# Performance work log

Measured on AMD Instinct MI355X. Metric: run time of the kernel, lower is better.

The kernel has to match this reference:

```python
import jax, jax.numpy as jnp
import numpy as np

V, E, H, K, B, T = 50000, 256, 512, 12, 32, 256
START, STOP = 10, 11
NEG = -10000.0
Hd = H // 2


def _lstm(x, h0, c0, Wih, Whh, bih, bhh):
    # x: [T, B, D] -> hidden states [T, B, Hd]; PyTorch gate order i,f,g,o
    def step(carry, xt):
        h, c = carry
        g = xt @ Wih.T + bih + h @ Whh.T + bhh
        i, f, gg, o = jnp.split(g, 4, axis=-1)
        c = jax.nn.sigmoid(f) * c + jax.nn.sigmoid(i) * jnp.tanh(gg)
        h = jax.nn.sigmoid(o) * jnp.tanh(c)
        return (h, c), h
    _, hs = jax.lax.scan(step, (h0, c0), x)
    return hs


def setup_inputs() -> dict:
    key = jax.random.key(0)
    ks = jax.random.split(key, 12)
    inp = {}
    inp["sentence"] = jax.random.randint(ks[0], (B, T), 0, V, dtype=jnp.int32)
    lens = jax.random.randint(ks[1], (B,), 1, T + 1, dtype=jnp.int32)
    inp["seq_lens"] = jnp.sort(lens)[::-1]  # pack_padded requires descending
    emb = jax.random.normal(ks[2], (V, E)) * 0.05
    inp["emb"] = emb.at[0].set(0.0)  # padding_idx=0
    def lw(k):
        a, b, c, d = jax.random.split(k, 4)
        return (jax.random.normal(a, (4 * Hd, E)) * 0.05,
                jax.random.normal(b, (4 * Hd, Hd)) * 0.05,
                jax.random.normal(c, (4 * Hd,)) * 0.05,
                jax.random.normal(d, (4 * Hd,)) * 0.05)
    inp["Wih_f"], inp["Whh_f"], inp["bih_f"], inp["bhh_f"] = lw(ks[3])
    inp["Wih_b"], inp["Whh_b"], inp["bih_b"], inp["bhh_b"] = lw(ks[4])
    inp["h0"] = jax.random.normal(ks[5], (2, B, Hd))  # init_hidden uses randn
    inp["c0"] = jax.random.normal(ks[6], (2, B, Hd))
    inp["W_out"] = jax.random.normal(ks[7], (K, H)) * 0.05
    inp["b_out"] = jax.random.normal(ks[8], (K,)) * 0.05
    trans = jax.random.normal(ks[9], (K, K))
    inp["transitions"] = trans.at[START, :].set(NEG).at[:, STOP].set(NEG)
    return inp


def _features(sentence, seq_lens, emb, Wih_f, Whh_f, bih_f, bhh_f,
              Wih_b, Whh_b, bih_b, bhh_b, h0, c0, W_out, b_out):
    x = emb[sentence]                       # [B,T,E]
    t_idx = jnp.arange(T)
    # forward direction
    hf = _lstm(x.transpose(1, 0, 2), h0[0], c0[0], Wih_f, Whh_f, bih_f, bhh_f)
    hf = hf.transpose(1, 0, 2)              # [B,T,Hd]
    # backward direction: reverse each sequence within its length (packed semantics)
    rev_idx = jnp.where(t_idx[None, :] < seq_lens[:, None],
                        seq_lens[:, None] - 1 - t_idx[None, :], t_idx[None, :])  # [B,T]
    x_rev = jnp.take_along_axis(x, rev_idx[:, :, None], axis=1)
    hb_rev = _lstm(x_rev.transpose(1, 0, 2), h0[1], c0[1], Wih_b, Whh_b, bih_b, bhh_b)
    hb = jnp.take_along_axis(hb_rev.transpose(1, 0, 2), rev_idx[:, :, None], axis=1)
    hcat = jnp.concatenate([hf, hb], axis=-1)  # [B,T,H]
    return hcat @ W_out.T + b_out              # [B,T,K]


def _viterbi(feats, seq_lens, transitions):
    t_idx = jnp.arange(T)
    mask = t_idx[None, :] < seq_lens[:, None]           # [B,T]
    init = jnp.full((B, K), NEG).at[:, START].set(0.0)  # forward_var

    def vstep(fv, inputs):
        feat_t, m_t = inputs                            # [B,K], [B]
        scores = fv[:, None, :] + transitions[None, :, :]   # [B, next, prev]
        bp = jnp.argmax(scores, axis=-1)                # [B,K]
        best = jnp.max(scores, axis=-1) + feat_t
        return jnp.where(m_t[:, None], best, fv), bp

    fv, bps = jax.lax.scan(vstep, init, (feats.transpose(1, 0, 2), mask.T))
    terminal = fv + transitions[STOP][None, :]          # [B,K]
    best_last = jnp.argmax(terminal, axis=-1)           # [B]
    path_scores = jnp.take_along_axis(terminal, best_last[:, None], axis=1)[:, 0]

    def btstep(tag, inputs):
        bp_t, m_t = inputs
        pred_t = jnp.where(m_t, tag, -1)
        prev = jnp.take_along_axis(bp_t, tag[:, None], axis=1)[:, 0]
        return jnp.where(m_t, prev, tag), pred_t

    _, preds_rev = jax.lax.scan(btstep, best_last, (bps[::-1], mask.T[::-1]))
    preds = preds_rev[::-1].transpose(1, 0)             # [B,T], -1 past seq_len
    return path_scores, preds


def reference(sentence, seq_lens, emb, Wih_f, Whh_f, bih_f, bhh_f,
              Wih_b, Whh_b, bih_b, bhh_b, h0, c0, W_out, b_out, transitions):
    feats = _features(sentence, seq_lens, emb, Wih_f, Whh_f, bih_f, bhh_f,
                      Wih_b, Whh_b, bih_b, bhh_b, h0, c0, W_out, b_out)
    scores, preds = _viterbi(feats, seq_lens, transitions)
    return scores, preds
```

## Files before the change

kernel.cpp:

```cpp
#include <hip/hip_runtime.h>
#include <math.h>

#define T_ 256
#define B_ 32
#define E_ 256
#define HD_ 256
#define NG_ 1024
#define K_ 12
#define START_ 10
#define STOP_ 11
#define NEG_ -10000.0f
#define MAGICU 0x40000000u
#define HSW(r) ((r) ^ (((r) >> 3) & 7))

typedef float f4_t __attribute__((ext_vector_type(4)));

__device__ __forceinline__ float sigf(float x) { return 1.0f / (1.0f + expf(-x)); }

__global__ void tok_gather(const int* __restrict__ sent, const int* __restrict__ lens,
                           int* __restrict__ tokA) {
    int e = blockIdx.x * 256 + threadIdx.x;
    int dir = e >> 13, m = e & 8191, t = m >> 5, b = m & 31;
    int len = lens[b];
    int tt = dir ? (t < len ? len - 1 - t : t) : t;
    tokA[e] = sent[b * T_ + tt];
}

__global__ void whh_tr(const float* __restrict__ Wf, const float* __restrict__ Wb,
                       float* __restrict__ WT) {
    int dir = blockIdx.x >> 8, k = blockIdx.x & 255, u = threadIdx.x;
    const float* W = dir ? Wb : Wf;
    float4 v;
    v.x = W[(0 * HD_ + u) * HD_ + k];
    v.y = W[(1 * HD_ + u) * HD_ + k];
    v.z = W[(2 * HD_ + u) * HD_ + k];
    v.w = W[(3 * HD_ + u) * HD_ + k];
    ((float4*)(WT + ((size_t)dir * 256 + k) * NG_))[u] = v;
}

__global__ void hex_init(float* __restrict__ hex) {
    int i = blockIdx.x * 256 + threadIdx.x;
    float4 m = make_float4(2.0f, 2.0f, 2.0f, 2.0f);
    ((float4*)hex)[i] = m;
}

__global__ __launch_bounds__(256) void in_gemm(
    const float* __restrict__ emb, const int* __restrict__ tokA,
    const float* __restrict__ Wih_f, const float* __restrict__ Wih_b,
    const float* __restrict__ bih_f, const float* __restrict__ bhh_f,
    const float* __restrict__ bih_b, const float* __restrict__ bhh_b,
    float* __restrict__ G) {
    const int dir = blockIdx.z;
    const int n0 = blockIdx.x * 128, m0 = blockIdx.y * 128;
    const float* Wih = dir ? Wih_b : Wih_f;
    const float* bihp = dir ? bih_b : bih_f;
    const float* bhhp = dir ? bhh_b : bhh_f;
    __shared__ float As[8][128];
    __shared__ float Bs[8][128];
    const int tid = threadIdx.x;
    const int rs = tid >> 1, kc = (tid & 1) * 4;
    const int tok = tokA[dir * 8192 + m0 + rs];
    const float* arow = emb + (size_t)tok * E_;
    const int np = n0 + rs;
    const int wrow = ((np & 3) << 8) | (np >> 2);
    const float* brow = Wih + (size_t)wrow * E_;
    const int ty = tid >> 4, tx = tid & 15;

    float acc[8][8];
#pragma unroll
    for (int i = 0; i < 8; ++i)
#pragma unroll
        for (int j = 0; j < 8; ++j) acc[i][j] = 0.f;

    for (int k0 = 0; k0 < E_; k0 += 8) {
        float4 av = *(const float4*)(arow + k0 + kc);
        float4 bv = *(const float4*)(brow + k0 + kc);
        __syncthreads();
        As[kc + 0][rs] = av.x; As[kc + 1][rs] = av.y; As[kc + 2][rs] = av.z; As[kc + 3][rs] = av.w;
        Bs[kc + 0][rs] = bv.x; Bs[kc + 1][rs] = bv.y; Bs[kc + 2][rs] = bv.z; Bs[kc + 3][rs] = bv.w;
        __syncthreads();
#pragma unroll
        for (int k = 0; k < 8; ++k) {
            float4 a0 = *(const float4*)&As[k][ty * 8];
            float4 a1 = *(const float4*)&As[k][ty * 8 + 4];
            float4 b0 = *(const float4*)&Bs[k][tx * 8];
            float4 b1 = *(const float4*)&Bs[k][tx * 8 + 4];
            float af8[8] = {a0.x, a0.y, a0.z, a0.w, a1.x, a1.y, a1.z, a1.w};
            float bf8[8] = {b0.x, b0.y, b0.z, b0.w, b1.x, b1.y, b1.z, b1.w};
#pragma unroll
            for (int i = 0; i < 8; ++i)
#pragma unroll
                for (int j = 0; j < 8; ++j) acc[i][j] += af8[i] * bf8[j];
        }
    }
    float bias[8];
#pragma unroll
    for (int j = 0; j < 8; ++j) {
        int nn = n0 + tx * 8 + j;
        int wr = ((nn & 3) << 8) | (nn >> 2);
        bias[j] = bihp[wr] + bhhp[wr];
    }
#pragma unroll
    for (int i = 0; i < 8; ++i) {
        int m = m0 + ty * 8 + i;
        float* gp = G + ((size_t)dir * 8192 + m) * NG_ + n0 + tx * 8;
        float4 o0 = {acc[i][0] + bias[0], acc[i][1] + bias[1], acc[i][2] + bias[2], acc[i][3] + bias[3]};
        float4 o1 = {acc[i][4] + bias[4], acc[i][5] + bias[5], acc[i][6] + bias[6], acc[i][7] + bias[7]};
        *(float4*)gp = o0;
        *(float4*)(gp + 4) = o1;
    }
}

__global__ __launch_bounds__(512, 1) void lstm_rec16(
    const float* __restrict__ WhhT, const float* __restrict__ G,
    const float* __restrict__ h0, const float* __restrict__ c0,
    const int* __restrict__ lens, float* __restrict__ hex) {
    const int wg = blockIdx.x;
    const int dir = wg >> 7, bt = (wg >> 5) & 3, ut = wg & 31;
    const int tid = threadIdx.x;
    const int wv = tid >> 6, ln = tid & 63;
    const int bh = wv >> 2;
    const int kq = wv & 3;
    const int u  = ln & 7;
    const int ks8 = kq * 8 + (ln >> 3);
    const int sb = bh * 4 + (ln & 3);
    const int sk = kq * 64 + (ln >> 2) * 4;
    const int speer = sk >> 3;

    __shared__ float4 hsA4[256];
    __shared__ float4 hsB4[256];
    __shared__ float4 red4[512 * 10];
    __shared__ float4 hT4[16];

    const int Tmax = lens[bt * 8];

    const float4* WT4 = (const float4*)(WhhT + (size_t)dir * 256 * NG_);
    const int gu = ut * 8 + u;
    float4 Wr[8];
#pragma unroll
    for (int j = 0; j < 8; ++j) Wr[j] = WT4[(ks8 * 8 + j) * 256 + gu];

    const bool is_act = (ln < 8);
    float c = 0.f;
    float4 gpend = make_float4(0.f, 0.f, 0.f, 0.f);
    const float* Gd = G + (size_t)dir * 8192 * NG_;
    if (is_act) {
        c = c0[(dir * B_ + bt * 8 + wv) * HD_ + gu];
        gpend = ((const float4*)(Gd + (size_t)(bt * 8 + wv) * NG_))[gu];
    }

    float* hexg = hex + (size_t)(dir * 4 + bt) * T_ * 2048;
    float4* hsX4 = bh ? hsB4 : hsA4;
    float* hsX = (float*)hsX4;

    f4_t pend;

    for (int t = 0; t < Tmax; ++t) {
        float4 hv;
        if (t == 0) {
            hv = *(const float4*)(h0 + (size_t)(dir * B_ + bt * 8 + sb) * HD_ + sk);
        } else if (speer == ut) {
            hv = hT4[sb * 2 + ((sk & 7) >> 2)];
        } else {
            asm volatile("s_waitcnt vmcnt(0)" ::: "memory");
            hv.x = pend.x; hv.y = pend.y; hv.z = pend.z; hv.w = pend.w;
            if (__float_as_uint(hv.x) == MAGICU || __float_as_uint(hv.y) == MAGICU ||
                __float_as_uint(hv.z) == MAGICU || __float_as_uint(hv.w) == MAGICU) {
                const float* src = hexg + (size_t)(t - 1) * 2048 + sb * 256 + sk;
                int it = 0;
                for (;;) {
                    __builtin_amdgcn_s_sleep(1);
                    float a0 = __hip_atomic_load(src + 0, __ATOMIC_RELAXED, __HIP_MEMORY_SCOPE_AGENT);
                    float a1 = __hip_atomic_load(src + 1, __ATOMIC_RELAXED, __HIP_MEMORY_SCOPE_AGENT);
                    float a2 = __hip_atomic_load(src + 2, __ATOMIC_RELAXED, __HIP_MEMORY_SCOPE_AGENT);
                    float a3 = __hip_atomic_load(src + 3, __ATOMIC_RELAXED, __HIP_MEMORY_SCOPE_AGENT);
                    if (!(__float_as_uint(a0) == MAGICU || __float_as_uint(a1) == MAGICU ||
                          __float_as_uint(a2) == MAGICU || __float_as_uint(a3) == MAGICU)) {
                        hv = make_float4(a0, a1, a2, a3); break;
                    }
                    if (++it > (1 << 22)) break;
                }
            }
        }
        hsX[HSW(sk + 0) * 4 + (ln & 3)] = hv.x;
        hsX[HSW(sk + 1) * 4 + (ln & 3)] = hv.y;
        hsX[HSW(sk + 2) * 4 + (ln & 3)] = hv.z;
        hsX[HSW(sk + 3) * 4 + (ln & 3)] = hv.w;
        asm volatile("s_waitcnt lgkmcnt(0)" ::: "memory");

        float4 a0 = {0,0,0,0}, a1 = {0,0,0,0}, a2 = {0,0,0,0}, a3 = {0,0,0,0};
#pragma unroll
        for (int j = 0; j < 8; ++j) {
            float4 h4 = hsX4[HSW(ks8 * 8 + j)];
            float4 w4 = Wr[j];
            a0.x += w4.x*h4.x; a0.y += w4.y*h4.x; a0.z += w4.z*h4.x; a0.w += w4.w*h4.x;
            a1.x += w4.x*h4.y; a1.y += w4.y*h4.y; a1.z += w4.z*h4.y; a1.w += w4.w*h4.y;
            a2.x += w4.x*h4.z; a2.y += w4.y*h4.z; a2.z += w4.z*h4.z; a2.w += w4.w*h4.z;
            a3.x += w4.x*h4.w; a3.y += w4.y*h4.w; a3.z += w4.z*h4.w; a3.w += w4.w*h4.w;
        }
        {
            float4* r = &red4[tid * 10];
            r[0] = a0; r[1] = a1; r[2] = a2; r[3] = a3;
        }
        asm volatile("s_waitcnt lgkmcnt(0)\n\ts_barrier" ::: "memory");

        if (is_act) {
            const int b = wv, bq = b & 3, bh2 = b >> 2;
            float si = gpend.x, sf = gpend.y, sg = gpend.z, so = gpend.w;
#pragma unroll
            for (int kq2 = 0; kq2 < 4; ++kq2)
#pragma unroll
                for (int ks2 = 0; ks2 < 8; ++ks2) {
                    int tid2 = ((bh2 * 4 + kq2) * 8 + ks2) * 8 + ln;
                    float4 p = red4[tid2 * 10 + bq];
                    si += p.x; sf += p.y; sg += p.z; so += p.w;
                }
            c = sigf(sf) * c + sigf(si) * tanhf(sg);
            float h = sigf(so) * tanhf(c);
            ((float*)hT4)[b * 8 + ln] = h;
            float* dst = hexg + (size_t)t * 2048 + b * 256 + gu;
            asm volatile("global_store_dword %0, %1, off sc0 sc1" :: "v"(dst), "v"(h) : "memory");
            if (t + 1 < Tmax)
                gpend = ((const float4*)(Gd + ((size_t)(t + 1) * B_ + bt * 8 + b) * NG_))[gu];
        }
        if (t + 1 < Tmax && speer != ut) {
            const float* nsrc = hexg + (size_t)t * 2048 + sb * 256 + sk;
            asm volatile("global_load_dwordx4 %0, %1, off sc0 sc1"
                         : "=v"(pend) : "v"(nsrc) : "memory");
        }
        asm volatile("s_waitcnt lgkmcnt(0)\n\ts_barrier" ::: "memory");
    }
}

__global__ void feat_k(const float* __restrict__ hex, const int* __restrict__ lens,
                       const float* __restrict__ Wout, const float* __restrict__ bout,
                       float* __restrict__ feats) {
    int tid = threadIdx.x;
    int pl = tid / 12, k = tid % 12;
    int p = blockIdx.x * 16 + pl;
    int b = p >> 8, t = p & 255;
    int len = lens[b];
    int tr = t < len ? len - 1 - t : t;
    const float4* hf = (const float4*)(hex + ((size_t)(b >> 3) * T_ + t) * 2048 + (b & 7) * 256);
    const float4* hb = (const float4*)(hex + ((size_t)(4 + (b >> 3)) * T_ + tr) * 2048 + (b & 7) * 256);
    const float4* w0 = (const float4*)(Wout + (size_t)k * 512);
    const float4* w1 = (const float4*)(Wout + (size_t)k * 512 + 256);
    float acc = bout[k];
#pragma unroll 4
    for (int j = 0; j < 64; ++j) {
        float4 h4 = hf[j], v4 = w0[j];
        acc += h4.x * v4.x + h4.y * v4.y + h4.z * v4.z + h4.w * v4.w;
    }
#pragma unroll 4
    for (int j = 0; j < 64; ++j) {
        float4 h4 = hb[j], v4 = w1[j];
        acc += h4.x * v4.x + h4.y * v4.y + h4.z * v4.z + h4.w * v4.w;
    }
    feats[(size_t)p * K_ + k] = acc;
}

__global__ __launch_bounds__(512) void viterbi_k(
    const float* __restrict__ feats, const float* __restrict__ trans,
    const int* __restrict__ lens, float* __restrict__ out) {
    __shared__ float fv[2][B_][16];
    __shared__ float tl[K_][16];
    __shared__ unsigned char bp[T_][B_][6];
    __shared__ int best_last[B_];
    int tid = threadIdx.x;
    int b = tid >> 4, lane = tid & 15;
    if (tid < K_ * K_) tl[tid / 12][tid % 12] = trans[tid];
    if (lane < K_) fv[0][b][lane] = (lane == START_) ? 0.f : NEG_;
    __syncthreads();
    int len = lens[b];
    int pp = 0;
    float f_cur = 0.f;
    if (lane < K_) f_cur = feats[(size_t)b * T_ * K_ + lane];
    for (int t = 0; t < T_; ++t) {
        float f_nxt = 0.f;
        if (t + 1 < T_ && lane < K_) f_nxt = feats[((size_t)b * T_ + t + 1) * K_ + lane];
        if (lane < K_) {
            float best = fv[pp][b][0] + tl[lane][0];
            int argp = 0;
#pragma unroll
            for (int p = 1; p < K_; ++p) {
                float v = fv[pp][b][p] + tl[lane][p];
                if (v > best) { best = v; argp = p; }
            }
            float nb = best + f_cur;
            fv[pp ^ 1][b][lane] = (t < len) ? nb : fv[pp][b][lane];
            int other = __shfl_xor(argp, 1);
            if ((lane & 1) == 0) bp[t][b][lane >> 1] = (unsigned char)(argp | (other << 4));
        }
        __syncthreads();
        pp ^= 1;
        f_cur = f_nxt;
    }
    if (lane == 0) {
        float best = fv[pp][b][0] + tl[STOP_][0];
        int bl = 0;
#pragma unroll
        for (int p = 1; p < K_; ++p) {
            float v = fv[pp][b][p] + tl[STOP_][p];
            if (v > best) { best = v; bl = p; }
        }
        out[b] = best;
        best_last[b] = bl;
    }
    __syncthreads();
    if (lane == 0) {
        int tag = best_last[b];
        for (int t = T_ - 1; t >= 0; --t) {
            int m = (t < len);
            out[B_ + b * T_ + t] = (float)(m ? tag : -1);
            if (m) tag = (bp[t][b][tag >> 1] >> ((tag & 1) * 4)) & 15;
        }
    }
}

extern "C" void kernel_launch(void* const* d_in, const int* in_sizes, int n_in,
                              void* d_out, int out_size, void* d_ws, size_t ws_size,
                              hipStream_t stream) {
    const int*   sent  = (const int*)d_in[0];
    const int*   lens  = (const int*)d_in[1];
    const float* emb   = (const float*)d_in[2];
    const float* Wih_f = (const float*)d_in[3];
    const float* Whh_f = (const float*)d_in[4];
    const float* bih_f = (const float*)d_in[5];
    const float* bhh_f = (const float*)d_in[6];
    const float* Wih_b = (const float*)d_in[7];
    const float* Whh_b = (const float*)d_in[8];
    const float* bih_b = (const float*)d_in[9];
    const float* bhh_b = (const float*)d_in[10];
    const float* h0    = (const float*)d_in[11];
    const float* c0    = (const float*)d_in[12];
    const float* Wout  = (const float*)d_in[13];
    const float* bout  = (const float*)d_in[14];
    const float* trans = (const float*)d_in[15];
    float* out = (float*)d_out;

    char* ws = (char*)d_ws;
    int*   tokA  = (int*)ws;
    float* WhhT  = (float*)(ws + 65536);
    float* G     = (float*)(ws + 2162688);
    float* feats = (float*)(ws + 69271552);
    float* hex   = (float*)(ws + 69664768);

    tok_gather<<<64, 256, 0, stream>>>(sent, lens, tokA);
    whh_tr<<<512, 256, 0, stream>>>(Whh_f, Whh_b, WhhT);
    hex_init<<<4096, 256, 0, stream>>>(hex);
    in_gemm<<<dim3(8, 64, 2), 256, 0, stream>>>(emb, tokA, Wih_f, Wih_b,
                                                bih_f, bhh_f, bih_b, bhh_b, G);
    lstm_rec16<<<256, 512, 0, stream>>>(WhhT, G, h0, c0, lens, hex);
    feat_k<<<512, 192, 0, stream>>>(hex, lens, Wout, bout, feats);
    viterbi_k<<<1, 512, 0, stream>>>(feats, trans, lens, out);
}
```

Before: 1.213 ms.

## Merge both LSTM directions into one workgroup with wider unit tiles

The recurrent LSTM kernel now uses 64 workgroups instead of 256. Each workgroup handles 16 hidden units (up from 8) and processes both the forward and backward directions, interleaved within each timestep. Keeping both directions' weights in registers means each workgroup exchanges hidden state with 15 peers instead of 31. Interleaving lets one direction's cross-workgroup load latency hide behind the other direction's compute. In exchange, register pressure doubles, there are twice as many barriers per step, and the vmcnt waits are hand-tuned and fragile.

New measurement: 1.636 ms. 1.35x slower.

```diff
diff --git a/kernel.cpp b/kernel.cpp
--- a/kernel.cpp
+++ b/kernel.cpp
@@ -11,7 +11,7 @@
 #define STOP_ 11
 #define NEG_ -10000.0f
 #define MAGICU 0x40000000u
-#define HSW(r) ((r) ^ (((r) >> 3) & 7))
+#define ISM(x) (__float_as_uint(x) == MAGICU)
 
 typedef float f4_t __attribute__((ext_vector_type(4)));
 
@@ -111,122 +111,206 @@
     }
 }
 
-__global__ __launch_bounds__(512, 1) void lstm_rec16(
+__global__ __launch_bounds__(512, 1) void lstm_recm(
     const float* __restrict__ WhhT, const float* __restrict__ G,
     const float* __restrict__ h0, const float* __restrict__ c0,
     const int* __restrict__ lens, float* __restrict__ hex) {
     const int wg = blockIdx.x;
-    const int dir = wg >> 7, bt = (wg >> 5) & 3, ut = wg & 31;
+    const int bt = wg >> 4, ut = wg & 15;
     const int tid = threadIdx.x;
     const int wv = tid >> 6, ln = tid & 63;
-    const int bh = wv >> 2;
-    const int kq = wv & 3;
-    const int u  = ln & 7;
-    const int ks8 = kq * 8 + (ln >> 3);
+    const int bh = wv >> 2, ksup = wv & 3;
+    const int kssub = ln >> 4, u = ln & 15;
+    const int ks = ksup * 4 + kssub;
+    const int gu = ut * 16 + u;
     const int sb = bh * 4 + (ln & 3);
-    const int sk = kq * 64 + (ln >> 2) * 4;
-    const int speer = sk >> 3;
+    const int sk = ksup * 64 + ((ln >> 2) & 15) * 4;
+    const int x4 = (sk >> 4) & 3;
+    const int speer = sk >> 4;
 
     __shared__ float4 hsA4[256];
     __shared__ float4 hsB4[256];
-    __shared__ float4 red4[512 * 10];
-    __shared__ float4 hT4[16];
+    __shared__ float4 red4[512 * 5];
+    __shared__ float4 hT4[2][32];
 
     const int Tmax = lens[bt * 8];
 
-    const float4* WT4 = (const float4*)(WhhT + (size_t)dir * 256 * NG_);
-    const int gu = ut * 8 + u;
-    float4 Wr[8];
-#pragma unroll
-    for (int j = 0; j < 8; ++j) Wr[j] = WT4[(ks8 * 8 + j) * 256 + gu];
-
-    const bool is_act = (ln < 8);
-    float c = 0.f;
-    float4 gpend = make_float4(0.f, 0.f, 0.f, 0.f);
-    const float* Gd = G + (size_t)dir * 8192 * NG_;
+    const float4* WT4 = (const float4*)WhhT;
+    float4 W0[16], W1[16];
+#pragma unroll
+    for (int j = 0; j < 16; ++j) {
+        W0[j] = WT4[(ks * 16 + j) * 256 + gu];
+        W1[j] = WT4[65536 + (ks * 16 + j) * 256 + gu];
+    }
+
+    const bool is_act = (ln < 16);
+    float cc0 = 0.f, cc1 = 0.f;
+    f4_t gp0, gp1;
+    const float* Gd0 = G;
+    const float* Gd1 = G + (size_t)8192 * NG_;
     if (is_act) {
-        c = c0[(dir * B_ + bt * 8 + wv) * HD_ + gu];
-        gpend = ((const float4*)(Gd + (size_t)(bt * 8 + wv) * NG_))[gu];
-    }
-
-    float* hexg = hex + (size_t)(dir * 4 + bt) * T_ * 2048;
+        cc0 = c0[(bt * 8 + wv) * HD_ + gu];
+        cc1 = c0[(B_ + bt * 8 + wv) * HD_ + gu];
+        gp0 = ((const f4_t*)(Gd0 + (size_t)(bt * 8 + wv) * NG_))[gu];
+        gp1 = ((const f4_t*)(Gd1 + (size_t)(bt * 8 + wv) * NG_))[gu];
+    }
+
+    float* hexg0 = hex + (size_t)bt * T_ * 2048;
+    float* hexg1 = hex + (size_t)(4 + bt) * T_ * 2048;
     float4* hsX4 = bh ? hsB4 : hsA4;
     float* hsX = (float*)hsX4;
 
-    f4_t pend;
+    f4_t pend0, pend1;
 
     for (int t = 0; t < Tmax; ++t) {
-        float4 hv;
-        if (t == 0) {
-            hv = *(const float4*)(h0 + (size_t)(dir * B_ + bt * 8 + sb) * HD_ + sk);
-        } else if (speer == ut) {
-            hv = hT4[sb * 2 + ((sk & 7) >> 2)];
-        } else {
-            asm volatile("s_waitcnt vmcnt(0)" ::: "memory");
-            hv.x = pend.x; hv.y = pend.y; hv.z = pend.z; hv.w = pend.w;
-            if (__float_as_uint(hv.x) == MAGICU || __float_as_uint(hv.y) == MAGICU ||
-                __float_as_uint(hv.z) == MAGICU || __float_as_uint(hv.w) == MAGICU) {
-                const float* src = hexg + (size_t)(t - 1) * 2048 + sb * 256 + sk;
-                int it = 0;
-                for (;;) {
-                    __builtin_amdgcn_s_sleep(1);
-                    float a0 = __hip_atomic_load(src + 0, __ATOMIC_RELAXED, __HIP_MEMORY_SCOPE_AGENT);
-                    float a1 = __hip_atomic_load(src + 1, __ATOMIC_RELAXED, __HIP_MEMORY_SCOPE_AGENT);
-                    float a2 = __hip_atomic_load(src + 2, __ATOMIC_RELAXED, __HIP_MEMORY_SCOPE_AGENT);
-                    float a3 = __hip_atomic_load(src + 3, __ATOMIC_RELAXED, __HIP_MEMORY_SCOPE_AGENT);
-                    if (!(__float_as_uint(a0) == MAGICU || __float_as_uint(a1) == MAGICU ||
-                          __float_as_uint(a2) == MAGICU || __float_as_uint(a3) == MAGICU)) {
-                        hv = make_float4(a0, a1, a2, a3); break;
+        {
+            float4 hv;
+            if (t == 0) {
+                hv = *(const float4*)(h0 + (size_t)(bt * 8 + sb) * HD_ + sk);
+            } else if (speer == ut) {
+                hv = hT4[0][sb * 4 + ((sk & 15) >> 2)];
+            } else {
+                asm volatile("s_waitcnt vmcnt(3)" : "+v"(pend0), "+v"(gp0) :: "memory");
+                hv.x = pend0.x; hv.y = pend0.y; hv.z = pend0.z; hv.w = pend0.w;
+                if (ISM(hv.x) || ISM(hv.y) || ISM(hv.z) || ISM(hv.w)) {
+                    const float* src = hexg0 + (size_t)(t - 1) * 2048 + sb * 256 + sk;
+                    int it = 0;
+                    for (;;) {
+                        __builtin_amdgcn_s_sleep(1);
+                        float a0 = __hip_atomic_load(src + 0, __ATOMIC_RELAXED, __HIP_MEMORY_SCOPE_AGENT);
+                        float a1 = __hip_atomic_load(src + 1, __ATOMIC_RELAXED, __HIP_MEMORY_SCOPE_AGENT);
+                        float a2 = __hip_atomic_load(src + 2, __ATOMIC_RELAXED, __HIP_MEMORY_SCOPE_AGENT);
+                        float a3 = __hip_atomic_load(src + 3, __ATOMIC_RELAXED, __HIP_MEMORY_SCOPE_AGENT);
+                        if (!(ISM(a0) || ISM(a1) || ISM(a2) || ISM(a3))) {
+                            hv = make_float4(a0, a1, a2, a3); break;
+                        }
+                        if (++it > (1 << 22)) break;
                     }
-                    if (++it > (1 << 22)) break;
                 }
             }
-        }
-        hsX[HSW(sk + 0) * 4 + (ln & 3)] = hv.x;
-        hsX[HSW(sk + 1) * 4 + (ln & 3)] = hv.y;
-        hsX[HSW(sk + 2) * 4 + (ln & 3)] = hv.z;
-        hsX[HSW(sk + 3) * 4 + (ln & 3)] = hv.w;
-        asm volatile("s_waitcnt lgkmcnt(0)" ::: "memory");
-
-        float4 a0 = {0,0,0,0}, a1 = {0,0,0,0}, a2 = {0,0,0,0}, a3 = {0,0,0,0};
-#pragma unroll
-        for (int j = 0; j < 8; ++j) {
-            float4 h4 = hsX4[HSW(ks8 * 8 + j)];
-            float4 w4 = Wr[j];
-            a0.x += w4.x*h4.x; a0.y += w4.y*h4.x; a0.z += w4.z*h4.x; a0.w += w4.w*h4.x;
-            a1.x += w4.x*h4.y; a1.y += w4.y*h4.y; a1.z += w4.z*h4.y; a1.w += w4.w*h4.y;
-            a2.x += w4.x*h4.z; a2.y += w4.y*h4.z; a2.z += w4.z*h4.z; a2.w += w4.w*h4.z;
-            a3.x += w4.x*h4.w; a3.y += w4.y*h4.w; a3.z += w4.z*h4.w; a3.w += w4.w*h4.w;
-        }
-        {
-            float4* r = &red4[tid * 10];
-            r[0] = a0; r[1] = a1; r[2] = a2; r[3] = a3;
+            hsX[(sk + (0 ^ x4)) * 4 + (ln & 3)] = hv.x;
+            hsX[(sk + (1 ^ x4)) * 4 + (ln & 3)] = hv.y;
+            hsX[(sk + (2 ^ x4)) * 4 + (ln & 3)] = hv.z;
+            hsX[(sk + (3 ^ x4)) * 4 + (ln & 3)] = hv.w;
+            asm volatile("s_waitcnt lgkmcnt(0)" ::: "memory");
+
+            float4 A0 = {0,0,0,0}, A1 = {0,0,0,0}, A2 = {0,0,0,0}, A3 = {0,0,0,0};
+#pragma unroll
+            for (int j = 0; j < 16; ++j) {
+                float4 h4 = hsX4[ks * 16 + (j ^ kssub)];
+                float4 w4 = W0[j];
+                A0.x += w4.x*h4.x; A0.y += w4.y*h4.x; A0.z += w4.z*h4.x; A0.w += w4.w*h4.x;
+                A1.x += w4.x*h4.y; A1.y += w4.y*h4.y; A1.z += w4.z*h4.y; A1.w += w4.w*h4.y;
+                A2.x += w4.x*h4.z; A2.y += w4.y*h4.z; A2.z += w4.z*h4.z; A2.w += w4.w*h4.z;
+                A3.x += w4.x*h4.w; A3.y += w4.y*h4.w; A3.z += w4.z*h4.w; A3.w += w4.w*h4.w;
+            }
+            float4* r = &red4[tid * 5];
+            r[(0 + kssub) & 3] = A0; r[(1 + kssub) & 3] = A1;
+            r[(2 + kssub) & 3] = A2; r[(3 + kssub) & 3] = A3;
         }
         asm volatile("s_waitcnt lgkmcnt(0)\n\ts_barrier" ::: "memory");
-
         if (is_act) {
-            const int b = wv, bq = b & 3, bh2 = b >> 2;
-            float si = gpend.x, sf = gpend.y, sg = gpend.z, so = gpend.w;
-#pragma unroll
-            for (int kq2 = 0; kq2 < 4; ++kq2)
-#pragma unroll
-                for (int ks2 = 0; ks2 < 8; ++ks2) {
-                    int tid2 = ((bh2 * 4 + kq2) * 8 + ks2) * 8 + ln;
-                    float4 p = red4[tid2 * 10 + bq];
+            const int b = wv, bq = b & 3, bhv = b >> 2;
+            float si = gp0.x, sf = gp0.y, sg = gp0.z, so = gp0.w;
+#pragma unroll
+            for (int k2 = 0; k2 < 4; ++k2)
+#pragma unroll
+                for (int k3 = 0; k3 < 4; ++k3) {
+                    int tid2 = (bhv * 4 + k2) * 64 + k3 * 16 + ln;
+                    float4 p = red4[tid2 * 5 + ((bq + k3) & 3)];
                     si += p.x; sf += p.y; sg += p.z; so += p.w;
                 }
-            c = sigf(sf) * c + sigf(si) * tanhf(sg);
-            float h = sigf(so) * tanhf(c);
-            ((float*)hT4)[b * 8 + ln] = h;
-            float* dst = hexg + (size_t)t * 2048 + b * 256 + gu;
+            cc0 = sigf(sf) * cc0 + sigf(si) * tanhf(sg);
+            float h = sigf(so) * tanhf(cc0);
+            ((float*)hT4[0])[b * 16 + ln] = h;
+            float* dst = hexg0 + (size_t)t * 2048 + b * 256 + gu;
             asm volatile("global_store_dword %0, %1, off sc0 sc1" :: "v"(dst), "v"(h) : "memory");
-            if (t + 1 < Tmax)
-                gpend = ((const float4*)(Gd + ((size_t)(t + 1) * B_ + bt * 8 + b) * NG_))[gu];
+            if (t + 1 < Tmax) {
+                const float* gsrc = Gd0 + ((size_t)(t + 1) * B_ + bt * 8 + b) * NG_ + (size_t)gu * 4;
+                asm volatile("global_load_dwordx4 %0, %1, off" : "=v"(gp0) : "v"(gsrc) : "memory");
+            }
         }
         if (t + 1 < Tmax && speer != ut) {
-            const float* nsrc = hexg + (size_t)t * 2048 + sb * 256 + sk;
+            const float* nsrc = hexg0 + (size_t)t * 2048 + sb * 256 + sk;
             asm volatile("global_load_dwordx4 %0, %1, off sc0 sc1"
-                         : "=v"(pend) : "v"(nsrc) : "memory");
+                         : "=v"(pend0) : "v"(nsrc) : "memory");
+        }
+        asm volatile("s_waitcnt lgkmcnt(0)\n\ts_barrier" ::: "memory");
+
+        {
+            float4 hv;
+            if (t == 0) {
+                hv = *(const float4*)(h0 + (size_t)(B_ + bt * 8 + sb) * HD_ + sk);
+            } else if (speer == ut) {
+                hv = hT4[1][sb * 4 + ((sk & 15) >> 2)];
+            } else {
+                if (t + 1 < Tmax)
+                    asm volatile("s_waitcnt vmcnt(3)" : "+v"(pend1), "+v"(gp1) :: "memory");
+                else
+                    asm volatile("s_waitcnt vmcnt(1)" : "+v"(pend1), "+v"(gp1) :: "memory");
+                hv.x = pend1.x; hv.y = pend1.y; hv.z = pend1.z; hv.w = pend1.w;
+                if (ISM(hv.x) || ISM(hv.y) || ISM(hv.z) || ISM(hv.w)) {
+                    const float* src = hexg1 + (size_t)(t - 1) * 2048 + sb * 256 + sk;
+                    int it = 0;
+                    for (;;) {
+                        __builtin_amdgcn_s_sleep(1);
+                        float a0 = __hip_atomic_load(src + 0, __ATOMIC_RELAXED, __HIP_MEMORY_SCOPE_AGENT);
+                        float a1 = __hip_atomic_load(src + 1, __ATOMIC_RELAXED, __HIP_MEMORY_SCOPE_AGENT);
+                        float a2 = __hip_atomic_load(src + 2, __ATOMIC_RELAXED, __HIP_MEMORY_SCOPE_AGENT);
+                        float a3 = __hip_atomic_load(src + 3, __ATOMIC_RELAXED, __HIP_MEMORY_SCOPE_AGENT);
+                        if (!(ISM(a0) || ISM(a1) || ISM(a2) || ISM(a3))) {
+                            hv = make_float4(a0, a1, a2, a3); break;
+                        }
+                        if (++it > (1 << 22)) break;
+                    }
+                }
+            }
+            hsX[(sk + (0 ^ x4)) * 4 + (ln & 3)] = hv.x;
+            hsX[(sk + (1 ^ x4)) * 4 + (ln & 3)] = hv.y;
+            hsX[(sk + (2 ^ x4)) * 4 + (ln & 3)] = hv.z;
+            hsX[(sk + (3 ^ x4)) * 4 + (ln & 3)] = hv.w;
+            asm volatile("s_waitcnt lgkmcnt(0)" ::: "memory");
+
+            float4 A0 = {0,0,0,0}, A1 = {0,0,0,0}, A2 = {0,0,0,0}, A3 = {0,0,0,0};
+#pragma unroll
+            for (int j = 0; j < 16; ++j) {
+                float4 h4 = hsX4[ks * 16 + (j ^ kssub)];
+                float4 w4 = W1[j];
+                A0.x += w4.x*h4.x; A0.y += w4.y*h4.x; A0.z += w4.z*h4.x; A0.w += w4.w*h4.x;
+                A1.x += w4.x*h4.y; A1.y += w4.y*h4.y; A1.z += w4.z*h4.y; A1.w += w4.w*h4.y;
+                A2.x += w4.x*h4.z; A2.y += w4.y*h4.z; A2.z += w4.z*h4.z; A2.w += w4.w*h4.z;
+                A3.x += w4.x*h4.w; A3.y += w4.y*h4.w; A3.z += w4.z*h4.w; A3.w += w4.w*h4.w;
+            }
+            float4* r = &red4[tid * 5];
+            r[(0 + kssub) & 3] = A0; r[(1 + kssub) & 3] = A1;
+            r[(2 + kssub) & 3] = A2; r[(3 + kssub) & 3] = A3;
+        }
+        asm volatile("s_waitcnt lgkmcnt(0)\n\ts_barrier" ::: "memory");
+        if (is_act) {
+            const int b = wv, bq = b & 3, bhv = b >> 2;
+            float si = gp1.x, sf = gp1.y, sg = gp1.z, so = gp1.w;
+#pragma unroll
+            for (int k2 = 0; k2 < 4; ++k2)
+#pragma unroll
+                for (int k3 = 0; k3 < 4; ++k3) {
+                    int tid2 = (bhv * 4 + k2) * 64 + k3 * 16 + ln;
+                    float4 p = red4[tid2 * 5 + ((bq + k3) & 3)];
+                    si += p.x; sf += p.y; sg += p.z; so += p.w;
+                }
+            cc1 = sigf(sf) * cc1 + sigf(si) * tanhf(sg);
+            float h = sigf(so) * tanhf(cc1);
+            ((float*)hT4[1])[b * 16 + ln] = h;
+            float* dst = hexg1 + (size_t)t * 2048 + b * 256 + gu;
+            asm volatile("global_store_dword %0, %1, off sc0 sc1" :: "v"(dst), "v"(h) : "memory");
+            if (t + 1 < Tmax) {
+                const float* gsrc = Gd1 + ((size_t)(t + 1) * B_ + bt * 8 + b) * NG_ + (size_t)gu * 4;
+                asm volatile("global_load_dwordx4 %0, %1, off" : "=v"(gp1) : "v"(gsrc) : "memory");
+            }
+        }
+        if (t + 1 < Tmax && speer != ut) {
+            const float* nsrc = hexg1 + (size_t)t * 2048 + sb * 256 + sk;
+            asm volatile("global_load_dwordx4 %0, %1, off sc0 sc1"
+                         : "=v"(pend1) : "v"(nsrc) : "memory");
         }
         asm volatile("s_waitcnt lgkmcnt(0)\n\ts_barrier" ::: "memory");
     }
@@ -350,7 +434,7 @@
     hex_init<<<4096, 256, 0, stream>>>(hex);
     in_gemm<<<dim3(8, 64, 2), 256, 0, stream>>>(emb, tokA, Wih_f, Wih_b,
                                                 bih_f, bhh_f, bih_b, bhh_b, G);
-    lstm_rec16<<<256, 512, 0, stream>>>(WhhT, G, h0, c0, lens, hex);
+    lstm_recm<<<64, 512, 0, stream>>>(WhhT, G, h0, c0, lens, hex);
     feat_k<<<512, 192, 0, stream>>>(hex, lens, Wout, bout, feats);
     viterbi_k<<<1, 512, 0, stream>>>(feats, trans, lens, out);
 }
```
